# Kernel optimization log

Measured on AMD Instinct MI355X. Metric: run time of the kernel, lower is better.

Reference implementation:

```python
import jax, jax.numpy as jnp
import numpy as np

B, T, N_OBS, H, N_ACT = 128, 512, 256, 512, 32


def setup_inputs() -> dict:
    key = jax.random.key(0)
    ks = jax.random.split(key, 9)
    s = lambda fan_in: 1.0 / np.sqrt(fan_in)
    return {
        "obs_seq": jax.random.normal(ks[0], (B, T, N_OBS), jnp.float32),
        "h0": jax.random.normal(ks[1], (B, H), jnp.float32),
        "c0": jax.random.normal(ks[2], (B, H), jnp.float32),
        "Wx": jax.random.normal(ks[3], (N_OBS, 4 * H), jnp.float32) * s(N_OBS),
        "Wh": jax.random.normal(ks[4], (H, 4 * H), jnp.float32) * s(H),
        "b": jnp.zeros((4 * H,), jnp.float32),
        "W1": jax.random.normal(ks[5], (H, 512), jnp.float32) * s(H),
        "b1": jnp.zeros((512,), jnp.float32),
        "W2": jax.random.normal(ks[6], (512, 512), jnp.float32) * s(512),
        "b2": jnp.zeros((512,), jnp.float32),
        "Wo": jax.random.normal(ks[7], (512, N_ACT), jnp.float32) * s(512),
        "bo": jnp.zeros((N_ACT,), jnp.float32),
        "action_min": jnp.zeros((N_ACT,), jnp.float32),
        "action_max": jnp.ones((N_ACT,), jnp.float32),
    }


def reference(obs_seq, h0, c0, Wx, Wh, b, W1, b1, W2, b2, Wo, bo, action_min, action_max):
    # Pre-compute input-to-gate projections for all timesteps in one big GEMM,
    # matching flax LSTMCell math: dense_i (no bias) on x, dense_h (bias) on h.
    xg = jnp.einsum('btf,fg->btg', obs_seq, Wx)  # (B, T, 4H)

    def step(carry, xg_t):
        h, c = carry
        z = xg_t + h @ Wh + b  # (B, 4H)
        i, f, g, o = jnp.split(z, 4, axis=-1)
        c = jax.nn.sigmoid(f) * c + jax.nn.sigmoid(i) * jnp.tanh(g)
        h = jax.nn.sigmoid(o) * jnp.tanh(c)
        return (h, c), h

    (h_T, c_T), ys = jax.lax.scan(step, (h0, c0), jnp.swapaxes(xg, 0, 1))
    x = jnp.swapaxes(ys, 0, 1)  # (B, T, H)

    x = jax.nn.relu(x @ W1 + b1)
    x = jax.nn.relu(x @ W2 + b2)
    x = jnp.tanh(x @ Wo + bo)
    action = 0.5 * (x * (action_max - action_min) + (action_max + action_min))
    return action, h_T, c_T
```

## Files before the change

kernel.cpp:

```cpp
#include <hip/hip_runtime.h>

typedef unsigned short u16;
typedef unsigned int u32;
typedef unsigned long long ull;
typedef __attribute__((ext_vector_type(8))) short bf16x8;
typedef __attribute__((ext_vector_type(4))) float f32x4;
typedef __attribute__((ext_vector_type(4))) unsigned u32x4;

#define B_   128
#define T_   512
#define NOBS 256
#define H_   512
#define G4   2048
#define NACT 32
#define M_   (B_*T_)
#define GR   8
#define ROWS 16
#define UN   16
#define ZW   66
#define SENT 0x7FC07FC0u

__device__ __forceinline__ float b2f(u16 s) {
  union { unsigned u; float f; } v; v.u = ((unsigned)s) << 16; return v.f;
}
__device__ __forceinline__ u16 f2b(float f) {
  union { float f; unsigned u; } v; v.f = f;
  unsigned r = v.u + 0x7FFFu + ((v.u >> 16) & 1u);
  return (u16)(r >> 16);
}
__device__ __forceinline__ float sigm(float x) { return 1.f/(1.f+__expf(-x)); }
__device__ __forceinline__ float tanh_f(float x) { return 1.f - 2.f/(1.f+__expf(2.f*x)); }

__device__ __forceinline__ void gld16(const void* g, void* ldsbase) {
#if __has_builtin(__builtin_amdgcn_global_load_lds)
  __builtin_amdgcn_global_load_lds((const __attribute__((address_space(1))) void*)g,
                                   (__attribute__((address_space(3))) void*)ldsbase, 16, 0, 0);
#else
  ((float4*)ldsbase)[threadIdx.x & 63] = *(const float4*)g;
#endif
}

__global__ void k_cvt_obsT(const float* __restrict__ in, u16* __restrict__ out) {
  const long i = (long)blockIdx.x*blockDim.x + threadIdx.x;
  const int k8 = (int)(i & (NOBS/8 - 1));
  const long row = i >> 5;
  const int t = (int)(row >> 7), b = (int)(row & (B_-1));
  const float* src = in + ((long)b*T_ + t)*NOBS + k8*8;
  ushort2 o[4];
  #pragma unroll
  for (int q = 0; q < 4; ++q) {
    o[q].x = f2b(src[q*2]);
    o[q].y = f2b(src[q*2+1]);
  }
  *(ushort2*)&out[i*8+0] = o[0]; *(ushort2*)&out[i*8+2] = o[1];
  *(ushort2*)&out[i*8+4] = o[2]; *(ushort2*)&out[i*8+6] = o[3];
}

__global__ void k_inith(const float* __restrict__ h0, u16* __restrict__ hp) {
  const int i = blockIdx.x*256 + threadIdx.x;
  const int plane = i >> 15, off = i & 32767;
  u32 v;
  if (plane == 0) {
    const int row = off >> 8, p = off & 255;
    v = (unsigned)f2b(h0[row*H_ + 2*p]) | ((unsigned)f2b(h0[row*H_ + 2*p + 1]) << 16);
  } else {
    v = SENT;
  }
  ((u32*)hp)[i] = v;
}

__global__ void k_transpose(const float* __restrict__ in, u16* __restrict__ out, int R, int C) {
  int i = blockIdx.x*blockDim.x + threadIdx.x;
  if (i < R*C) {
    int c = i / R, r = i - c*R;
    out[i] = f2b(in[r*C + c]);
  }
}

template<int EPI>
__global__ __launch_bounds__(256) void k_gemm_bt(const u16* __restrict__ A, const u16* __restrict__ BT,
                                                 u16* __restrict__ C, const float* __restrict__ bias,
                                                 int M, int N, int K)
{
  __shared__ u16 As[128*64];
  __shared__ u16 Bs[128*64];
  const int tid = threadIdx.x, wv = tid >> 6, lane = tid & 63;
  const int ntile = N >> 7;
  const int tm = blockIdx.x / ntile, tn = blockIdx.x - tm*ntile;
  const int wr = wv >> 1, wc = wv & 1;
  f32x4 acc[4][4];
  for (int m=0;m<4;++m) for (int n=0;n<4;++n) acc[m][n] = (f32x4){0.f,0.f,0.f,0.f};
  const long abase = (long)tm*128, bbase = (long)tn*128;
  const int kit = K >> 6;
  for (int kt = 0; kt < kit; ++kt) {
    const int k0 = kt << 6;
    #pragma unroll
    for (int q = 0; q < 4; ++q) {
      int off = (wv*4+q)*1024 + lane*16;
      int row = off >> 7, colb = off & 127;
      gld16((const char*)A  + ((abase+row)*K + k0)*2 + colb, (char*)As + (wv*4+q)*1024);
      gld16((const char*)BT + ((bbase+row)*K + k0)*2 + colb, (char*)Bs + (wv*4+q)*1024);
    }
    asm volatile("s_waitcnt vmcnt(0)" ::: "memory");
    __syncthreads();
    const int kg = (lane >> 4) * 8;
    #pragma unroll
    for (int kk = 0; kk < 64; kk += 32) {
      bf16x8 af[4], bfr[4];
      #pragma unroll
      for (int m = 0; m < 4; ++m)
        af[m] = *(const bf16x8*)(As + (wr*64 + m*16 + (lane&15))*64 + kk + kg);
      #pragma unroll
      for (int n = 0; n < 4; ++n)
        bfr[n] = *(const bf16x8*)(Bs + (wc*64 + n*16 + (lane&15))*64 + kk + kg);
      #pragma unroll
      for (int m = 0; m < 4; ++m)
        #pragma unroll
        for (int n = 0; n < 4; ++n)
          acc[m][n] = __builtin_amdgcn_mfma_f32_16x16x32_bf16(af[m], bfr[n], acc[m][n], 0, 0, 0);
    }
    __syncthreads();
  }
  const int rq = (lane >> 4) * 4, cl = lane & 15;
  #pragma unroll
  for (int n = 0; n < 4; ++n) {
    const int coln = (int)bbase + wc*64 + n*16 + cl;
    const float bv = (EPI == 1) ? bias[coln] : 0.f;
    #pragma unroll
    for (int m = 0; m < 4; ++m) {
      const long rowb = abase + wr*64 + m*16 + rq;
      #pragma unroll
      for (int q = 0; q < 4; ++q) {
        float v = acc[m][n][q];
        if (EPI == 1) v = fmaxf(v + bv, 0.f);
        C[(rowb+q)*(long)N + coln] = f2b(v);
      }
    }
  }
}

__global__ __launch_bounds__(256, 1) void k_scan(
    const u16* __restrict__ obsT, const u16* __restrict__ WxT, const u16* __restrict__ WhT,
    const float* __restrict__ bvec, const float* __restrict__ c0f,
    u16* __restrict__ hp,
    u16* __restrict__ ys, float* __restrict__ outh, float* __restrict__ outc)
{
  __shared__ float zs[2][16*ZW];
  __shared__ float cst[256];
  __shared__ float bsl[64];
  __shared__ char pad_[98304];

  const int tid = threadIdx.x, wv = tid >> 6, lane = tid & 63;
  const int wg = blockIdx.x, isl = wg & (GR-1), cg = wg >> 3;
  const int rb0 = isl*ROWS, S0 = cg*UN;
  ((volatile char*)pad_)[tid] = 0;

  const int kh = wv >> 1, ch = wv & 1;
  const int C0 = ch*32;
  const int lq = lane >> 4, l15 = lane & 15;
  const int arow = rb0 + l15;

  const int j0 = C0 + l15, j1 = j0 + 16;
  const long w0 = (long)((j0 >> 4)*H_ + S0 + (j0 & 15));
  const long w1 = (long)((j1 >> 4)*H_ + S0 + (j1 & 15));
  bf16x8 wbx[4][2], wbh[8][2];
  #pragma unroll
  for (int ks = 0; ks < 4; ++ks) {
    const long k = (long)kh*128 + ks*32 + lq*8;
    wbx[ks][0] = *(const bf16x8*)(WxT + w0*NOBS + k);
    wbx[ks][1] = *(const bf16x8*)(WxT + w1*NOBS + k);
  }
  #pragma unroll
  for (int ks = 0; ks < 8; ++ks) {
    const long k = (long)kh*256 + ks*32 + lq*8;
    wbh[ks][0] = *(const bf16x8*)(WhT + w0*H_ + k);
    wbh[ks][1] = *(const bf16x8*)(WhT + w1*H_ + k);
  }

  cst[tid] = c0f[(rb0 + (tid >> 4))*H_ + S0 + (tid & 15)];
  if (tid < 64) bsl[tid] = bvec[(tid >> 4)*H_ + S0 + (tid & 15)];
  __syncthreads();

  const long fofs = (long)arow*H_ + kh*256 + lq*8;

  bf16x8 ax[4];
  {
    const u16* Ax = obsT + (long)arow*NOBS + kh*128 + lq*8;
    #pragma unroll
    for (int ks = 0; ks < 4; ++ks) ax[ks] = *(const bf16x8*)(Ax + ks*32);
  }

  for (int t = 0; t < T_; ++t) {
    f32x4 acc0 = {0.f,0.f,0.f,0.f}, acc1 = {0.f,0.f,0.f,0.f};

    #pragma unroll
    for (int ks = 0; ks < 4; ++ks) {
      acc0 = __builtin_amdgcn_mfma_f32_16x16x32_bf16(ax[ks], wbx[ks][0], acc0, 0, 0, 0);
      acc1 = __builtin_amdgcn_mfma_f32_16x16x32_bf16(ax[ks], wbx[ks][1], acc1, 0, 0, 0);
    }

    union { u32x4 u; bf16x8 v; } hf[8];
    {
      const u16* haddr = hp + ((long)(t & 7) << 16) + fofs;
      asm volatile("s_waitcnt vmcnt(0)" ::: "memory");
      int spin = 1 << 12;
      for (;;) {
        #pragma unroll
        for (int ks = 0; ks < 8; ++ks)
          asm volatile("global_load_dwordx4 %0, %1, off offset:%2 sc0 sc1"
                       : "=v"(hf[ks].u) : "v"(haddr), "i"(ks*64));
        asm volatile("s_waitcnt vmcnt(0)" ::: "memory");
        __builtin_amdgcn_sched_barrier(0);
        unsigned ready = 1u;
        #pragma unroll
        for (int ks = 0; ks < 8; ++ks)
          #pragma unroll
          for (int j = 0; j < 4; ++j)
            ready &= (hf[ks].u[j] != SENT) ? 1u : 0u;
        if (__all((int)ready)) break;
        if (--spin == 0) break;
      }
    }

    bf16x8 axn[4];
    {
      const int tn = (t+1 < T_) ? t+1 : t;
      const u16* Axn = obsT + ((long)tn*B_ + arow)*NOBS + kh*128 + lq*8;
      #pragma unroll
      for (int ks = 0; ks < 4; ++ks) axn[ks] = *(const bf16x8*)(Axn + ks*32);
    }

    #pragma unroll
    for (int ks = 0; ks < 8; ++ks) {
      acc0 = __builtin_amdgcn_mfma_f32_16x16x32_bf16(hf[ks].v, wbh[ks][0], acc0, 0, 0, 0);
      acc1 = __builtin_amdgcn_mfma_f32_16x16x32_bf16(hf[ks].v, wbh[ks][1], acc1, 0, 0, 0);
    }
    #pragma unroll
    for (int ks = 0; ks < 4; ++ks) ax[ks] = axn[ks];

    {
      const int zr0 = lq*4, zc = C0 + l15;
      #pragma unroll
      for (int q = 0; q < 4; ++q) {
        zs[kh][(zr0+q)*ZW + zc]      = acc0[q];
        zs[kh][(zr0+q)*ZW + zc + 16] = acc1[q];
      }
    }
    __syncthreads();

    if (tid < 128) {
      const int rr = tid >> 3, pp = tid & 7;
      float hv2[2], cn2[2];
      #pragma unroll
      for (int u = 0; u < 2; ++u) {
        const int sl = 2*pp + u;
        const float* z0 = &zs[0][rr*ZW];
        const float* z1 = &zs[1][rr*ZW];
        const float zi = z0[sl]    + z1[sl]    + bsl[sl];
        const float zf = z0[16+sl] + z1[16+sl] + bsl[16+sl];
        const float zg = z0[32+sl] + z1[32+sl] + bsl[32+sl];
        const float zo = z0[48+sl] + z1[48+sl] + bsl[48+sl];
        const float cv = cst[rr*16 + sl];
        const float cn = sigm(zf)*cv + sigm(zi)*tanh_f(zg);
        hv2[u] = sigm(zo)*tanh_f(cn);
        cn2[u] = cn;
        cst[rr*16 + sl] = cn;
      }
      const unsigned h01 = (unsigned)f2b(hv2[0]) | ((unsigned)f2b(hv2[1]) << 16);
      const int bq = rb0 + rr;
      const long wofs = (long)bq*H_ + S0 + 2*pp;
      if (t < T_-1)
        __hip_atomic_store((u32*)(hp + ((long)((t+1) & 7) << 16) + wofs), h01,
                           __ATOMIC_RELAXED, __HIP_MEMORY_SCOPE_AGENT);
      __hip_atomic_store((u32*)(hp + ((long)((t+5) & 7) << 16) + wofs), SENT,
                         __ATOMIC_RELAXED, __HIP_MEMORY_SCOPE_AGENT);
      *(u32*)(ys + ((long)bq*T_ + t)*H_ + S0 + 2*pp) = h01;
      if (t == T_-1) {
        outh[bq*H_ + S0 + 2*pp]     = hv2[0];
        outh[bq*H_ + S0 + 2*pp + 1] = hv2[1];
        outc[bq*H_ + S0 + 2*pp]     = cn2[0];
        outc[bq*H_ + S0 + 2*pp + 1] = cn2[1];
      }
    }
  }
}

__global__ __launch_bounds__(256) void k_head(const u16* __restrict__ X, const u16* __restrict__ WoT,
    const float* __restrict__ bo, const float* __restrict__ amin, const float* __restrict__ amax,
    float* __restrict__ out)
{
  __shared__ u16 Ws[NACT*H_];
  __shared__ float sc[3*NACT];
  const int tid = threadIdx.x;
  #pragma unroll
  for (int q = 0; q < 8; ++q)
    ((float4*)Ws)[q*256 + tid] = ((const float4*)WoT)[q*256 + tid];
  if (tid < NACT) { sc[tid] = bo[tid]; sc[NACT+tid] = amin[tid]; sc[2*NACT+tid] = amax[tid]; }
  __syncthreads();
  const long r = (long)blockIdx.x*64 + (tid >> 2);
  const int c0 = (tid & 3)*8;
  float acc[8];
  #pragma unroll
  for (int c = 0; c < 8; ++c) acc[c] = 0.f;
  const u16* Arow = X + r*H_;
  for (int kc = 0; kc < H_/8; ++kc) {
    bf16x8 a = *(const bf16x8*)(Arow + kc*8);
    float av[8];
    #pragma unroll
    for (int j = 0; j < 8; ++j) av[j] = b2f((u16)a[j]);
    #pragma unroll
    for (int c = 0; c < 8; ++c) {
      bf16x8 w = *(const bf16x8*)(Ws + (c0+c)*H_ + kc*8);
      #pragma unroll
      for (int j = 0; j < 8; ++j) acc[c] += av[j] * b2f((u16)w[j]);
    }
  }
  #pragma unroll
  for (int c = 0; c < 8; ++c) {
    const int cc = c0 + c;
    const float y = acc[c] + sc[cc];
    const float tv = tanhf(y);
    out[r*NACT + cc] = 0.5f*(tv*(sc[2*NACT+cc]-sc[NACT+cc]) + (sc[2*NACT+cc]+sc[NACT+cc]));
  }
}

extern "C" void kernel_launch(void* const* d_in, const int* in_sizes, int n_in,
                              void* d_out, int out_size, void* d_ws, size_t ws_size,
                              hipStream_t stream) {
  const float* obs = (const float*)d_in[0];
  const float* h0  = (const float*)d_in[1];
  const float* c0  = (const float*)d_in[2];
  const float* Wx  = (const float*)d_in[3];
  const float* Wh  = (const float*)d_in[4];
  const float* bb  = (const float*)d_in[5];
  const float* W1  = (const float*)d_in[6];
  const float* b1  = (const float*)d_in[7];
  const float* W2  = (const float*)d_in[8];
  const float* b2  = (const float*)d_in[9];
  const float* Wo  = (const float*)d_in[10];
  const float* bo  = (const float*)d_in[11];
  const float* amin= (const float*)d_in[12];
  const float* amax= (const float*)d_in[13];

  char* ws = (char*)d_ws;
  u16* obsT  = (u16*)(ws + 0);
  u16* ys    = (u16*)(ws + 33554432);
  u16* t1    = (u16*)(ws + 100663296);
  u16* t2    = (u16*)(ws + 33554432);
  u16* hp    = (u16*)(ws + 100663296);
  u16* WxT   = (u16*)(ws + 167772160);
  u16* WhT   = (u16*)(ws + 168820736);
  u16* W1T   = (u16*)(ws + 170917888);
  u16* W2T   = (u16*)(ws + 171442176);
  u16* WoT   = (u16*)(ws + 171966464);

  float* outA = (float*)d_out;
  float* outh = outA + (long)M_*NACT;
  float* outc = outh + B_*H_;

  k_cvt_obsT<<<M_*NOBS/8/256, 256, 0, stream>>>(obs, obsT);
  k_inith<<<1024, 256, 0, stream>>>(h0, hp);
  k_transpose<<<2048, 256, 0, stream>>>(Wx, WxT, NOBS, G4);
  k_transpose<<<4096, 256, 0, stream>>>(Wh, WhT, H_, G4);
  k_transpose<<<1024, 256, 0, stream>>>(W1, W1T, H_, H_);
  k_transpose<<<1024, 256, 0, stream>>>(W2, W2T, H_, H_);
  k_transpose<<<64,   256, 0, stream>>>(Wo, WoT, H_, NACT);

  k_scan<<<256, 256, 0, stream>>>(obsT, WxT, WhT, bb, c0, hp, ys, outh, outc);

  k_gemm_bt<1><<<(M_/128)*(H_/128), 256, 0, stream>>>(ys, W1T, t1, b1, M_, H_, H_);
  k_gemm_bt<1><<<(M_/128)*(H_/128), 256, 0, stream>>>(t1, W2T, t2, b2, M_, H_, H_);
  k_head<<<M_/64, 256, 0, stream>>>(t2, WoT, bo, amin, amax, outA);
}
```

Baseline: 1.515 ms.

## Stage LSTM weights in LDS and issue h loads before x-projection MFMAs

Moves the per-block Wx/Wh weight slices from registers into a shared-memory buffer, which also replaces the dummy LDS padding that held occupancy down. Each timestep now issues the speculative h-state loads first, then does the input-projection MFMAs while those loads are in flight, and only enters the spin-wait loop if the first read still sees sentinels. This hides global latency on the recurrent critical path and frees many VGPRs. The cost is extra LDS reads per step, which may compete with MFMA issue.

After: 1.538 ms. About the same (+1.5%).

```diff
diff --git a/kernel.cpp b/kernel.cpp
--- a/kernel.cpp
+++ b/kernel.cpp
@@ -145,43 +145,33 @@
     u16* __restrict__ hp,
     u16* __restrict__ ys, float* __restrict__ outh, float* __restrict__ outc)
 {
+  __shared__ u16 Bw[96*64*8];
   __shared__ float zs[2][16*ZW];
   __shared__ float cst[256];
   __shared__ float bsl[64];
-  __shared__ char pad_[98304];
 
   const int tid = threadIdx.x, wv = tid >> 6, lane = tid & 63;
   const int wg = blockIdx.x, isl = wg & (GR-1), cg = wg >> 3;
   const int rb0 = isl*ROWS, S0 = cg*UN;
-  ((volatile char*)pad_)[tid] = 0;
 
   const int kh = wv >> 1, ch = wv & 1;
   const int C0 = ch*32;
   const int lq = lane >> 4, l15 = lane & 15;
   const int arow = rb0 + l15;
 
-  const int j0 = C0 + l15, j1 = j0 + 16;
-  const long w0 = (long)((j0 >> 4)*H_ + S0 + (j0 & 15));
-  const long w1 = (long)((j1 >> 4)*H_ + S0 + (j1 & 15));
-  bf16x8 wbx[4][2], wbh[8][2];
-  #pragma unroll
-  for (int ks = 0; ks < 4; ++ks) {
-    const long k = (long)kh*128 + ks*32 + lq*8;
-    wbx[ks][0] = *(const bf16x8*)(WxT + w0*NOBS + k);
-    wbx[ks][1] = *(const bf16x8*)(WxT + w1*NOBS + k);
-  }
-  #pragma unroll
-  for (int ks = 0; ks < 8; ++ks) {
-    const long k = (long)kh*256 + ks*32 + lq*8;
-    wbh[ks][0] = *(const bf16x8*)(WhT + w0*H_ + k);
-    wbh[ks][1] = *(const bf16x8*)(WhT + w1*H_ + k);
-  }
-
+  for (int idx = tid; idx < 96*64; idx += 256) {
+    const int kg = idx >> 6, col = idx & 63;
+    const long jrow = (long)((col >> 4)*H_ + S0 + (col & 15));
+    const u16* src = (kg < 32) ? (WxT + jrow*NOBS + kg*8)
+                               : (WhT + jrow*H_ + (long)(kg-32)*8);
+    *(bf16x8*)(Bw + (long)idx*8) = *(const bf16x8*)src;
+  }
   cst[tid] = c0f[(rb0 + (tid >> 4))*H_ + S0 + (tid & 15)];
   if (tid < 64) bsl[tid] = bvec[(tid >> 4)*H_ + S0 + (tid & 15)];
   __syncthreads();
 
   const long fofs = (long)arow*H_ + kh*256 + lq*8;
+  const int ldsC = (C0 + l15)*8;
 
   bf16x8 ax[4];
   {
@@ -192,33 +182,53 @@
 
   for (int t = 0; t < T_; ++t) {
     f32x4 acc0 = {0.f,0.f,0.f,0.f}, acc1 = {0.f,0.f,0.f,0.f};
+    union { u32x4 u; bf16x8 v; } hf[8];
+    const u16* haddr = hp + ((long)(t & 7) << 16) + fofs;
+
+    asm volatile("s_waitcnt vmcnt(0)" ::: "memory");
+
+    #pragma unroll
+    for (int ks = 0; ks < 8; ++ks)
+      asm volatile("global_load_dwordx4 %0, %1, off offset:%2 sc0 sc1"
+                   : "=v"(hf[ks].u) : "v"(haddr), "i"(ks*64));
 
     #pragma unroll
     for (int ks = 0; ks < 4; ++ks) {
-      acc0 = __builtin_amdgcn_mfma_f32_16x16x32_bf16(ax[ks], wbx[ks][0], acc0, 0, 0, 0);
-      acc1 = __builtin_amdgcn_mfma_f32_16x16x32_bf16(ax[ks], wbx[ks][1], acc1, 0, 0, 0);
-    }
-
-    union { u32x4 u; bf16x8 v; } hf[8];
+      const u16* bp = Bw + (kh*16 + ks*4 + lq)*512 + ldsC;
+      bf16x8 b0 = *(const bf16x8*)bp;
+      bf16x8 b1 = *(const bf16x8*)(bp + 128);
+      acc0 = __builtin_amdgcn_mfma_f32_16x16x32_bf16(ax[ks], b0, acc0, 0, 0, 0);
+      acc1 = __builtin_amdgcn_mfma_f32_16x16x32_bf16(ax[ks], b1, acc1, 0, 0, 0);
+    }
+    __builtin_amdgcn_sched_barrier(0);
+
     {
-      const u16* haddr = hp + ((long)(t & 7) << 16) + fofs;
       asm volatile("s_waitcnt vmcnt(0)" ::: "memory");
-      int spin = 1 << 12;
-      for (;;) {
+      __builtin_amdgcn_sched_barrier(0);
+      unsigned ready = 1u;
+      #pragma unroll
+      for (int ks = 0; ks < 8; ++ks)
         #pragma unroll
-        for (int ks = 0; ks < 8; ++ks)
-          asm volatile("global_load_dwordx4 %0, %1, off offset:%2 sc0 sc1"
-                       : "=v"(hf[ks].u) : "v"(haddr), "i"(ks*64));
-        asm volatile("s_waitcnt vmcnt(0)" ::: "memory");
-        __builtin_amdgcn_sched_barrier(0);
-        unsigned ready = 1u;
-        #pragma unroll
-        for (int ks = 0; ks < 8; ++ks)
+        for (int j = 0; j < 4; ++j)
+          ready &= (hf[ks].u[j] != SENT) ? 1u : 0u;
+      if (!__all((int)ready)) {
+        int spin = 1 << 12;
+        for (;;) {
           #pragma unroll
-          for (int j = 0; j < 4; ++j)
-            ready &= (hf[ks].u[j] != SENT) ? 1u : 0u;
-        if (__all((int)ready)) break;
-        if (--spin == 0) break;
+          for (int ks = 0; ks < 8; ++ks)
+            asm volatile("global_load_dwordx4 %0, %1, off offset:%2 sc0 sc1"
+                         : "=v"(hf[ks].u) : "v"(haddr), "i"(ks*64));
+          asm volatile("s_waitcnt vmcnt(0)" ::: "memory");
+          __builtin_amdgcn_sched_barrier(0);
+          unsigned rdy = 1u;
+          #pragma unroll
+          for (int ks = 0; ks < 8; ++ks)
+            #pragma unroll
+            for (int j = 0; j < 4; ++j)
+              rdy &= (hf[ks].u[j] != SENT) ? 1u : 0u;
+          if (__all((int)rdy)) break;
+          if (--spin == 0) break;
+        }
       }
     }
 
@@ -232,8 +242,11 @@
 
     #pragma unroll
     for (int ks = 0; ks < 8; ++ks) {
-      acc0 = __builtin_amdgcn_mfma_f32_16x16x32_bf16(hf[ks].v, wbh[ks][0], acc0, 0, 0, 0);
-      acc1 = __builtin_amdgcn_mfma_f32_16x16x32_bf16(hf[ks].v, wbh[ks][1], acc1, 0, 0, 0);
+      const u16* bp = Bw + (32 + kh*32 + ks*4 + lq)*512 + ldsC;
+      bf16x8 b0 = *(const bf16x8*)bp;
+      bf16x8 b1 = *(const bf16x8*)(bp + 128);
+      acc0 = __builtin_amdgcn_mfma_f32_16x16x32_bf16(hf[ks].v, b0, acc0, 0, 0, 0);
+      acc1 = __builtin_amdgcn_mfma_f32_16x16x32_bf16(hf[ks].v, b1, acc1, 0, 0, 0);
     }
     #pragma unroll
     for (int ks = 0; ks < 4; ++ks) ax[ks] = axn[ks];
```
